# Kernel tuning notes

Measured on AMD Instinct MI355X. Metric: run time of the kernel, lower is better.

The kernel has to match this reference:

```python
import jax, jax.numpy as jnp
import numpy as np

N_SRC = 50000
N_TGT = 50000
E = 320000
D = 256          # feature dim == hidden_channels
H = 256
OUT = 16
L = 2
P_DROP = 0.1
NEG_SLOPE = 0.01  # F.leaky_relu default


def _seg_mean(x, src_idx, dst_idx, n_dst):
    # gather source features along edges, mean-aggregate per destination (PyG SAGE default aggr='mean')
    msgs = x[src_idx]                                            # [E, D]
    s = jax.ops.segment_sum(msgs, dst_idx, num_segments=n_dst)   # [n_dst, D]
    cnt = jax.ops.segment_sum(jnp.ones((dst_idx.shape[0],), x.dtype), dst_idx, num_segments=n_dst)
    return s / jnp.maximum(cnt, 1.0)[:, None]


def _dropout(x, p, key):
    keep = jax.random.bernoulli(key, 1.0 - p, x.shape)
    return jnp.where(keep, x / (1.0 - p), jnp.zeros((), x.dtype))


def setup_inputs() -> dict:
    key = jax.random.key(0)
    ks = jax.random.split(key, 16)
    sc_in = 1.0 / np.sqrt(D)
    sc_h = 1.0 / np.sqrt(H)
    inp = {
        'x_source': jax.random.normal(ks[0], (N_SRC, D), jnp.float32),
        'x_target': jax.random.normal(ks[1], (N_TGT, D), jnp.float32),
        'ei_st': jax.random.randint(ks[2], (2, E), 0, N_SRC, jnp.int32),  # row0: source idx, row1: target idx
        'ei_ts': jax.random.randint(ks[3], (2, E), 0, N_TGT, jnp.int32),  # row0: target idx, row1: source idx
        # SAGEConv params per layer per relation; lin_l has bias, lin_r does not (PyG)
        'Wl_st': jax.random.normal(ks[4], (L, D, H), jnp.float32) * sc_in,
        'Wr_st': jax.random.normal(ks[5], (L, D, H), jnp.float32) * sc_in,
        'b_st': jnp.zeros((L, H), jnp.float32),
        'Wl_ts': jax.random.normal(ks[6], (L, D, H), jnp.float32) * sc_in,
        'Wr_ts': jax.random.normal(ks[7], (L, D, H), jnp.float32) * sc_in,
        'b_ts': jnp.zeros((L, H), jnp.float32),
        'Wout': jax.random.normal(ks[8], (H, OUT), jnp.float32) * sc_h,
        'bout': jnp.zeros((OUT,), jnp.float32),
    }
    return inp


def reference(x_source, x_target, ei_st, ei_ts, Wl_st, Wr_st, b_st, Wl_ts, Wr_ts, b_ts, Wout, bout):
    drop_key = jax.random.key(42)
    x_s, x_t = x_source, x_target
    for l in range(L):
        # relation ('source','edge','target'): messages source -> target
        m_t = _seg_mean(x_s, ei_st[0], ei_st[1], N_TGT)
        new_t = m_t @ Wl_st[l] + b_st[l] + x_t @ Wr_st[l]
        # relation ('target','rev_edge','source'): messages target -> source
        m_s = _seg_mean(x_t, ei_ts[0], ei_ts[1], N_SRC)
        new_s = m_s @ Wl_ts[l] + b_ts[l] + x_s @ Wr_ts[l]
        # leaky_relu + dropout (F.dropout default training=True)
        new_s = jnp.where(new_s >= 0, new_s, NEG_SLOPE * new_s)
        new_t = jnp.where(new_t >= 0, new_t, NEG_SLOPE * new_t)
        x_s = _dropout(new_s, P_DROP, jax.random.fold_in(drop_key, 2 * l))
        x_t = _dropout(new_t, P_DROP, jax.random.fold_in(drop_key, 2 * l + 1))
    return x_s @ Wout + bout  # [N_SRC, OUT]
```

## Files before the change

### kernel.cpp

```cpp
#include <hip/hip_runtime.h>
#include <stdint.h>

#define NSRC 50000
#define NTGT 50000
#define NE   320000
#define DIN  256
#define HID  256
#define DOUT 16

#define GBM 64
#define GBLK ((NSRC + GBM - 1) / GBM)
#define MASK_DW_PER (GBLK * 512)

typedef __attribute__((ext_vector_type(8))) short bf16x8;
typedef __attribute__((ext_vector_type(4))) float f32x4;

__device__ inline ushort f2b(float f) {
  uint32_t u = __float_as_uint(f);
  return (ushort)((u + 0x7FFFu + ((u >> 16) & 1u)) >> 16);
}
__device__ inline float b2f(ushort h) { return __uint_as_float(((uint32_t)h) << 16); }

typedef __attribute__((address_space(3))) uint32_t lds_u32_t;
typedef const __attribute__((address_space(1))) uint32_t glb_u32_t;
__device__ __forceinline__ void ld_lds16(const ushort* g, ushort* lds) {
  __builtin_amdgcn_global_load_lds((glb_u32_t*)g, (lds_u32_t*)lds, 16, 0, 0);
}

__host__ __device__ constexpr uint64_t tf2x32(uint32_t k0, uint32_t k1,
                                              uint32_t x0, uint32_t x1) {
  uint32_t ks2 = k0 ^ k1 ^ 0x1BD11BDAu;
  x0 += k0; x1 += k1;
#define TF_ROT(x, r) (((x) << (r)) | ((x) >> (32 - (r))))
#define TF_RND(r) { x0 += x1; x1 = TF_ROT(x1, r) ^ x0; }
  TF_RND(13) TF_RND(15) TF_RND(26) TF_RND(6)
  x0 += k1;  x1 += ks2 + 1u;
  TF_RND(17) TF_RND(29) TF_RND(16) TF_RND(24)
  x0 += ks2; x1 += k0 + 2u;
  TF_RND(13) TF_RND(15) TF_RND(26) TF_RND(6)
  x0 += k0;  x1 += k1 + 3u;
  TF_RND(17) TF_RND(29) TF_RND(16) TF_RND(24)
  x0 += k1;  x1 += ks2 + 4u;
  TF_RND(13) TF_RND(15) TF_RND(26) TF_RND(6)
  x0 += ks2; x1 += k0 + 5u;
#undef TF_RND
#undef TF_ROT
  return (uint64_t(x0) << 32) | uint64_t(x1);
}

constexpr uint64_t FOLD[4] = {
  tf2x32(0u, 42u, 0u, 0u),
  tf2x32(0u, 42u, 0u, 1u),
  tf2x32(0u, 42u, 0u, 2u),
  tf2x32(0u, 42u, 0u, 3u),
};

__device__ __forceinline__ void mask_word(uint32_t* __restrict__ masks, int d) {
  int g = d / MASK_DW_PER;
  int w = d - g * MASK_DW_PER;
  int gt = w >> 1, half = w & 1;
  int gblk = gt >> 8, gtid = gt & 255;
  int wave = gtid >> 6, lane = gtid & 63;
  int q = lane >> 4, r = lane & 15;
  uint64_t fk = (g == 0) ? FOLD[1] : (g == 1 ? FOLD[0] : FOLD[2]);
  uint32_t kk0 = (uint32_t)(fk >> 32), kk1 = (uint32_t)fk;
  int mbase = gblk * GBM;
  uint32_t mword = 0;
#pragma unroll
  for (int bb = 0; bb < 32; ++bb) {
    int s = half * 32 + bb;
    int si = s >> 4, se = (s >> 2) & 3, sj = s & 3;
    uint32_t rowg = (uint32_t)(mbase + si * 16 + q * 4 + se);
    uint32_t colg = (uint32_t)(wave * 64 + sj * 16 + r);
    uint64_t rr = tf2x32(kk0, kk1, 0u, rowg * 256u + colg);
    uint32_t bits = (uint32_t)(rr >> 32) ^ (uint32_t)rr;
    mword |= (((bits >> 9) < 7549747u) ? 1u : 0u) << bb;
  }
  masks[d] = mword;
}

#define NB_CVT  25000
#define NB_W    96
#define NB_HIST 2500
#define PREP_T  (NB_CVT + NB_W + NB_HIST)

struct PrepArgs {
  const float *xs, *xt;
  ushort *oxs, *oxt;
  const float* wsrc[6];
  ushort* wdst[6];
  const int *ei_a, *ei_b;
  int *cur_a, *cur_b;
};

__global__ __launch_bounds__(256) void prep_kernel(PrepArgs p) {
  __shared__ ushort tile[64][65];
  int blk = (int)(((long long)blockIdx.x * 97) % PREP_T);
  int tid = threadIdx.x;
  if (blk < NB_CVT) {
    const float* in = blk < (NB_CVT / 2) ? p.xs : p.xt;
    ushort* out = blk < (NB_CVT / 2) ? p.oxs : p.oxt;
    int i = (blk % (NB_CVT / 2)) * 256 + tid;
    float4 v = ((const float4*)in)[i];
    ushort4 o;
    o.x = f2b(v.x); o.y = f2b(v.y); o.z = f2b(v.z); o.w = f2b(v.w);
    ((ushort4*)out)[i] = o;
    return;
  }
  blk -= NB_CVT;
  if (blk < NB_W) {
    const float* W = p.wsrc[blk >> 4];
    ushort* Wt = p.wdst[blk >> 4];
    int ktile = (blk >> 2) & 3, ntile = blk & 3;
#pragma unroll
    for (int rep = 0; rep < 16; ++rep) {
      int lin = rep * 256 + tid;
      int kk = lin >> 6, nn = lin & 63;
      tile[nn][kk] = f2b(W[(size_t)(ktile * 64 + kk) * 256 + ntile * 64 + nn]);
    }
    __syncthreads();
#pragma unroll
    for (int rep = 0; rep < 16; ++rep) {
      int lin = rep * 256 + tid;
      int nn = lin >> 6, kk = lin & 63;
      Wt[(size_t)(ntile * 64 + nn) * 256 + ktile * 64 + kk] = tile[nn][kk];
    }
    return;
  }
  blk -= NB_W;
  const int* ei = blk < (NB_HIST / 2) ? p.ei_a : p.ei_b;
  int* cur = blk < (NB_HIST / 2) ? p.cur_a : p.cur_b;
  int e = (blk % (NB_HIST / 2)) * 256 + tid;
  if (e < NE) atomicAdd(cur + ei[NE + e], 1);
}

#define SB 1024
__global__ __launch_bounds__(SB) void scan_partial(const int* __restrict__ cur_a,
                                                   const int* __restrict__ cur_b,
                                                   int* __restrict__ bsum,
                                                   int n, int nbPer) {
  __shared__ int red[SB];
  int b = blockIdx.x;
  const int* cnt = b < nbPer ? cur_a : cur_b;
  int i = (b % nbPer) * SB + threadIdx.x;
  red[threadIdx.x] = (i < n) ? cnt[i] : 0;
  __syncthreads();
  for (int d = SB / 2; d > 0; d >>= 1) {
    if (threadIdx.x < d) red[threadIdx.x] += red[threadIdx.x + d];
    __syncthreads();
  }
  if (threadIdx.x == 0) bsum[b] = red[0];
}

__global__ __launch_bounds__(128) void scan_base(int* __restrict__ bsum, int nbPer) {
  __shared__ int buf[2][64];
  int half = threadIdx.x >> 6;
  int t = threadIdx.x & 63;
  buf[half][t] = (t < nbPer) ? bsum[half * nbPer + t] : 0;
  __syncthreads();
  for (int d = 1; d < 64; d <<= 1) {
    int v = (t >= d) ? buf[half][t - d] : 0;
    __syncthreads();
    buf[half][t] += v;
    __syncthreads();
  }
  if (t < nbPer) bsum[half * nbPer + t] = (t == 0) ? 0 : buf[half][t - 1];
}

__global__ __launch_bounds__(SB) void scan_final(int* __restrict__ cur_a,
                                                 int* __restrict__ cur_b,
                                                 int* __restrict__ offs_a,
                                                 int* __restrict__ offs_b,
                                                 const int* __restrict__ bsum,
                                                 int n, int nbPer) {
  __shared__ int part[SB];
  int b = blockIdx.x;
  bool first = b < nbPer;
  int* cur = first ? cur_a : cur_b;
  int* offs = first ? offs_a : offs_b;
  int i = (b % nbPer) * SB + threadIdx.x;
  int v = (i < n) ? cur[i] : 0;
  part[threadIdx.x] = v;
  __syncthreads();
  for (int d = 1; d < SB; d <<= 1) {
    int tv = (threadIdx.x >= d) ? part[threadIdx.x - d] : 0;
    __syncthreads();
    part[threadIdx.x] += tv;
    __syncthreads();
  }
  int excl = part[threadIdx.x] - v + bsum[b];
  if (i < n) {
    offs[i] = excl;
    cur[i] = 0;
  }
  if (i == n - 1) offs[n] = excl + v;
}

__global__ __launch_bounds__(256) void csr_fill2(const int* __restrict__ ei_a,
                                                 const int* __restrict__ ei_b,
                                                 const int* __restrict__ offs_a,
                                                 const int* __restrict__ offs_b,
                                                 int* __restrict__ cur_a,
                                                 int* __restrict__ cur_b,
                                                 int* __restrict__ adj_a,
                                                 int* __restrict__ adj_b,
                                                 int nE, int nbPer) {
  int blk = blockIdx.x;
  bool first = blk < nbPer;
  const int* ei = first ? ei_a : ei_b;
  const int* offs = first ? offs_a : offs_b;
  int* cur = first ? cur_a : cur_b;
  int* adj = first ? adj_a : adj_b;
  int e = (blk % nbPer) * 256 + threadIdx.x;
  if (e >= nE) return;
  int dst = ei[nE + e];
  int pos = atomicAdd(cur + dst, 1);
  adj[offs[dst] + pos] = ei[e];
}

__device__ __forceinline__ void gather_row(const ushort* __restrict__ x,
                                           const int* __restrict__ offs,
                                           const int* __restrict__ adj,
                                           ushort* __restrict__ m,
                                           int row, int lane) {
  int start = offs[row], end = offs[row + 1];
  float a0 = 0.f, a1 = 0.f, a2 = 0.f, a3 = 0.f;
  int e = start;
  for (; e + 3 < end; e += 4) {
    int s0 = adj[e], s1 = adj[e + 1], s2 = adj[e + 2], s3 = adj[e + 3];
    ushort4 v0 = *(const ushort4*)(x + (size_t)s0 * DIN + lane * 4);
    ushort4 v1 = *(const ushort4*)(x + (size_t)s1 * DIN + lane * 4);
    ushort4 v2 = *(const ushort4*)(x + (size_t)s2 * DIN + lane * 4);
    ushort4 v3 = *(const ushort4*)(x + (size_t)s3 * DIN + lane * 4);
    a0 += b2f(v0.x); a1 += b2f(v0.y); a2 += b2f(v0.z); a3 += b2f(v0.w);
    a0 += b2f(v1.x); a1 += b2f(v1.y); a2 += b2f(v1.z); a3 += b2f(v1.w);
    a0 += b2f(v2.x); a1 += b2f(v2.y); a2 += b2f(v2.z); a3 += b2f(v2.w);
    a0 += b2f(v3.x); a1 += b2f(v3.y); a2 += b2f(v3.z); a3 += b2f(v3.w);
  }
  for (; e < end; ++e) {
    int s = adj[e];
    ushort4 v = *(const ushort4*)(x + (size_t)s * DIN + lane * 4);
    a0 += b2f(v.x); a1 += b2f(v.y); a2 += b2f(v.z); a3 += b2f(v.w);
  }
  float inv = 1.0f / fmaxf((float)(end - start), 1.0f);
  ushort4 o;
  o.x = f2b(a0 * inv); o.y = f2b(a1 * inv); o.z = f2b(a2 * inv); o.w = f2b(a3 * inv);
  *(ushort4*)(m + (size_t)row * DIN + lane * 4) = o;
}

#define GG_GB 12500
#define G2_MASKB (2 * MASK_DW_PER / 256)
#define G2_T (2 * GG_GB + G2_MASKB)

__global__ __launch_bounds__(256) void gather2_mean_h(
    const ushort* __restrict__ xa, const int* __restrict__ offsa,
    const int* __restrict__ adja, ushort* __restrict__ ma,
    const ushort* __restrict__ xb, const int* __restrict__ offsb,
    const int* __restrict__ adjb, ushort* __restrict__ mb,
    uint32_t* __restrict__ masks, int nRows, int nbPer) {
  int blk = (int)(((long long)blockIdx.x * 97) % G2_T);
  int tid = threadIdx.x;
  if (blk >= 2 * nbPer) {
    mask_word(masks, (blk - 2 * nbPer) * 256 + tid);
    return;
  }
  bool first = blk < nbPer;
  int row = (blk % nbPer) * 4 + (tid >> 6);
  if (row >= nRows) return;
  if (first) gather_row(xa, offsa, adja, ma, row, tid & 63);
  else       gather_row(xb, offsb, adjb, mb, row, tid & 63);
}

__device__ __forceinline__ void gemm_body(
    int bid, const ushort* __restrict__ A1, const ushort* __restrict__ A2,
    const ushort* __restrict__ W1t, const ushort* __restrict__ W2t,
    const float* __restrict__ bias, const uint2* __restrict__ mk,
    ushort* __restrict__ C, int M, ushort* sA, ushort* sB) {
  const int tid = threadIdx.x;
  const int wave = tid >> 6, lane = tid & 63;
  const int q = lane >> 4, r = lane & 15;
  const int mbase = bid * GBM;

  const uint2 km = mk[bid * 256 + tid];

  f32x4 acc[4][4] = {};

  const int arow = tid >> 2;
  const int akc = (tid & 3) * 8;
  const int agrow = min(mbase + arow, M - 1);
  const ushort* a1p = A1 + (size_t)agrow * DIN + akc;
  const ushort* a2p = A2 + (size_t)agrow * DIN + akc;
  const ushort* w1b = W1t + (size_t)arow * DIN + akc;
  const ushort* w2b = W2t + (size_t)arow * DIN + akc;
  ushort* ldsA0 = sA + wave * 512;
  ushort* ldsA1 = sA + 2048 + wave * 512;

#pragma unroll
  for (int t = 0; t < 8; ++t) {
    const int kt = t * 32;
    __syncthreads();
    ld_lds16(a1p + kt, ldsA0);
    ld_lds16(a2p + kt, ldsA1);
#pragma unroll
    for (int c = 0; c < 4; ++c) {
      ld_lds16(w1b + c * (64 * DIN) + kt, sB + c * 2048 + wave * 512);
      ld_lds16(w2b + c * (64 * DIN) + kt, sB + 8192 + c * 2048 + wave * 512);
    }
    __syncthreads();
#pragma unroll
    for (int ph = 0; ph < 2; ++ph) {
      bf16x8 af[4], bfr[4];
#pragma unroll
      for (int i = 0; i < 4; ++i)
        af[i] = *(const bf16x8*)&sA[ph * 2048 + (i * 16 + r) * 32 + q * 8];
#pragma unroll
      for (int j = 0; j < 4; ++j)
        bfr[j] = *(const bf16x8*)&sB[ph * 8192 + (wave * 64 + j * 16 + r) * 32 + q * 8];
#pragma unroll
      for (int i = 0; i < 4; ++i)
#pragma unroll
        for (int j = 0; j < 4; ++j)
          acc[i][j] = __builtin_amdgcn_mfma_f32_16x16x32_bf16(af[i], bfr[j],
                                                              acc[i][j], 0, 0, 0);
    }
  }

  float bj[4];
#pragma unroll
  for (int j = 0; j < 4; ++j) bj[j] = bias[wave * 64 + j * 16 + r];
#pragma unroll
  for (int i = 0; i < 4; ++i) {
#pragma unroll
    for (int e = 0; e < 4; ++e) {
      int rowg = mbase + i * 16 + q * 4 + e;
      if (rowg >= M) continue;
#pragma unroll
      for (int j = 0; j < 4; ++j) {
        const int s = i * 16 + e * 4 + j;
        int colg = wave * 64 + j * 16 + r;
        float v = acc[i][j][e] + bj[j];
        v = v >= 0.0f ? v : 0.01f * v;
        uint32_t keep = ((s < 32 ? km.x >> s : km.y >> (s - 32)) & 1u);
        v = keep ? v * (1.0f / 0.9f) : 0.0f;
        C[(size_t)rowg * HID + colg] = f2b(v);
      }
    }
  }
}

__global__ __launch_bounds__(256, 4) void gemm_dual_mfma(
    const ushort* __restrict__ A1, const ushort* __restrict__ A2,
    const ushort* __restrict__ W1t, const ushort* __restrict__ W2t,
    const float* __restrict__ bias, const uint2* __restrict__ mk,
    ushort* __restrict__ C, int M) {
  __shared__ ushort sA[2][GBM * 32];
  __shared__ ushort sB[2][HID * 32];
  gemm_body(blockIdx.x, A1, A2, W1t, W2t, bias, mk, C, M, &sA[0][0], &sB[0][0]);
}

#define GG_MASKB (MASK_DW_PER / 256)
#define GG_T  (GBLK + GG_GB + GG_MASKB)

__global__ __launch_bounds__(256, 4) void gemm_gather(
    const ushort* __restrict__ A1, const ushort* __restrict__ A2,
    const ushort* __restrict__ W1t, const ushort* __restrict__ W2t,
    const float* __restrict__ bias, const uint2* __restrict__ mk,
    ushort* __restrict__ C, int M,
    const ushort* __restrict__ gx, const int* __restrict__ goffs,
    const int* __restrict__ gadj, ushort* __restrict__ gm, int gRows,
    uint32_t* __restrict__ masks) {
  __shared__ ushort sA[2][GBM * 32];
  __shared__ ushort sB[2][HID * 32];
  int blk = (int)(((long long)blockIdx.x * 101) % GG_T);
  if (blk < GBLK) {
    gemm_body(blk, A1, A2, W1t, W2t, bias, mk, C, M, &sA[0][0], &sB[0][0]);
  } else if (blk < GBLK + GG_GB) {
    int row = (blk - GBLK) * 4 + (threadIdx.x >> 6);
    if (row < gRows) gather_row(gx, goffs, gadj, gm, row, threadIdx.x & 63);
  } else {
    mask_word(masks,
              2 * MASK_DW_PER + (blk - GBLK - GG_GB) * 256 + (int)threadIdx.x);
  }
}

__global__ __launch_bounds__(256) void out_gemm_h(const ushort* __restrict__ X,
                                                  const float* __restrict__ Wout,
                                                  const float* __restrict__ bout,
                                                  float* __restrict__ C, int M) {
  __shared__ float sW[DIN * DOUT];
  int tid = threadIdx.x;
#pragma unroll
  for (int i = 0; i < (DIN * DOUT) / 256; ++i) sW[i * 256 + tid] = Wout[i * 256 + tid];
  __syncthreads();
  int rr = tid >> 4, c = tid & 15;
  int row = blockIdx.x * 16 + rr;
  if (row >= M) return;
  float acc = bout[c];
  const ushort* xp = X + (size_t)row * DIN;
  for (int k = 0; k < DIN; k += 8) {
    uint4 u = *(const uint4*)(xp + k);
    const ushort* us = (const ushort*)&u;
#pragma unroll
    for (int t = 0; t < 8; ++t) acc += b2f(us[t]) * sW[(k + t) * DOUT + c];
  }
  C[(size_t)row * DOUT + c] = acc;
}

extern "C" void kernel_launch(void* const* d_in, const int* in_sizes, int n_in,
                              void* d_out, int out_size, void* d_ws, size_t ws_size,
                              hipStream_t stream) {
  const float* x_source = (const float*)d_in[0];
  const float* x_target = (const float*)d_in[1];
  const int* ei_st = (const int*)d_in[2];
  const int* ei_ts = (const int*)d_in[3];
  const float* Wl_st = (const float*)d_in[4];
  const float* Wr_st = (const float*)d_in[5];
  const float* b_st  = (const float*)d_in[6];
  const float* Wl_ts = (const float*)d_in[7];
  const float* Wr_ts = (const float*)d_in[8];
  const float* b_ts  = (const float*)d_in[9];
  const float* Wout  = (const float*)d_in[10];
  const float* bout  = (const float*)d_in[11];
  float* out = (float*)d_out;

  const size_t F = (size_t)NSRC * DIN;
  const size_t WM = (size_t)DIN * HID;
  const int nbScan = (NSRC + SB - 1) / SB;
  const size_t intCount = (NTGT + 1) + (NSRC + 1) + 2 * NE + NTGT + NSRC +
                          2 * nbScan + 3 * MASK_DW_PER;
  const size_t need = (5 * F + 6 * WM) * sizeof(ushort) + intCount * sizeof(int);
  if (ws_size < need) return;

  ushort* xs0h = (ushort*)d_ws;
  ushort* xt0h = xs0h + F;
  ushort* B0h  = xt0h + F;
  ushort* B1h  = B0h + F;
  ushort* B2h  = B1h + F;
  ushort* wt0  = B2h + F;
  ushort* wt1  = wt0 + WM;
  ushort* wt2  = wt1 + WM;
  ushort* wt3  = wt2 + WM;
  ushort* wt4  = wt3 + WM;
  ushort* wt5  = wt4 + WM;
  int* ip      = (int*)(wt5 + WM);
  int* offs_st = ip;
  int* offs_ts = offs_st + NTGT + 1;
  int* adj_st  = offs_ts + NSRC + 1;
  int* adj_ts  = adj_st + NE;
  int* cur_t   = adj_ts + NE;
  int* cur_s   = cur_t + NTGT;
  int* bsum    = cur_s + NSRC;
  uint32_t* masks = (uint32_t*)(bsum + 2 * nbScan);

  const int EB = (NE + 255) / 256;
  const int GGB = NTGT / 4;

  hipMemsetAsync(cur_t, 0, (NTGT + NSRC) * sizeof(int), stream);
  PrepArgs pa;
  pa.xs = x_source; pa.xt = x_target; pa.oxs = xs0h; pa.oxt = xt0h;
  pa.wsrc[0] = Wl_st;      pa.wdst[0] = wt0;
  pa.wsrc[1] = Wr_st;      pa.wdst[1] = wt1;
  pa.wsrc[2] = Wl_ts;      pa.wdst[2] = wt2;
  pa.wsrc[3] = Wr_ts;      pa.wdst[3] = wt3;
  pa.wsrc[4] = Wl_ts + WM; pa.wdst[4] = wt4;
  pa.wsrc[5] = Wr_ts + WM; pa.wdst[5] = wt5;
  pa.ei_a = ei_st; pa.ei_b = ei_ts;
  pa.cur_a = cur_t; pa.cur_b = cur_s;
  prep_kernel<<<PREP_T, 256, 0, stream>>>(pa);

  scan_partial<<<2 * nbScan, SB, 0, stream>>>(cur_t, cur_s, bsum, NTGT, nbScan);
  scan_base<<<1, 128, 0, stream>>>(bsum, nbScan);
  scan_final<<<2 * nbScan, SB, 0, stream>>>(cur_t, cur_s, offs_st, offs_ts,
                                            bsum, NTGT, nbScan);
  csr_fill2<<<2 * EB, 256, 0, stream>>>(ei_st, ei_ts, offs_st, offs_ts,
                                        cur_t, cur_s, adj_st, adj_ts, NE, EB);

  gather2_mean_h<<<G2_T, 256, 0, stream>>>(xs0h, offs_st, adj_st, B0h,
                                           xt0h, offs_ts, adj_ts, B1h,
                                           masks, NTGT, GGB);

  gemm_dual_mfma<<<GBLK, 256, 0, stream>>>(
      B0h, xt0h, wt0, wt1, b_st, (const uint2*)(masks), B2h, NTGT);

  gemm_gather<<<GG_T, 256, 0, stream>>>(
      B1h, xs0h, wt2, wt3, b_ts, (const uint2*)(masks + MASK_DW_PER), B0h, NSRC,
      B2h, offs_ts, adj_ts, xt0h, NSRC, masks);

  gemm_dual_mfma<<<GBLK, 256, 0, stream>>>(
      xt0h, B0h, wt4, wt5, b_ts + HID, (const uint2*)(masks + 2 * MASK_DW_PER),
      B2h, NSRC);

  out_gemm_h<<<(NSRC + 15) / 16, 256, 0, stream>>>(B2h, Wout, bout, out, NSRC);
}
```

Baseline: 446.6 us.

## Fuse output projection into final GEMM and widen gather to 16-byte loads

The final dual GEMM now applies leaky_relu and dropout, writes the activated bf16 tile to swizzled LDS, and computes the 256x16 output projection in the same kernel. This removes the separate out_gemm kernel and the global round-trip of the last hidden activations. The mean-gather now uses 32 lanes per row with 16-byte loads, so each block covers 8 rows and the grid is halved. Mask and gather outputs use nontemporal stores. The risks are higher LDS use and register pressure in the fused kernel, and fewer in-flight rows per wave in the gather.

After: 544.8 us. 22.0% more time.

```diff
diff --git a/kernel.cpp b/kernel.cpp
--- a/kernel.cpp
+++ b/kernel.cpp
@@ -14,6 +14,7 @@
 
 typedef __attribute__((ext_vector_type(8))) short bf16x8;
 typedef __attribute__((ext_vector_type(4))) float f32x4;
+typedef __attribute__((ext_vector_type(4))) uint u32x4;
 
 __device__ inline ushort f2b(float f) {
   uint32_t u = __float_as_uint(f);
@@ -76,7 +77,7 @@
     uint32_t bits = (uint32_t)(rr >> 32) ^ (uint32_t)rr;
     mword |= (((bits >> 9) < 7549747u) ? 1u : 0u) << bb;
   }
-  masks[d] = mword;
+  __builtin_nontemporal_store(mword, masks + d);
 }
 
 #define NB_CVT  25000
@@ -218,37 +219,52 @@
   adj[offs[dst] + pos] = ei[e];
 }
 
-__device__ __forceinline__ void gather_row(const ushort* __restrict__ x,
-                                           const int* __restrict__ offs,
-                                           const int* __restrict__ adj,
-                                           ushort* __restrict__ m,
-                                           int row, int lane) {
+__device__ __forceinline__ void gather_row8(const ushort* __restrict__ x,
+                                            const int* __restrict__ offs,
+                                            const int* __restrict__ adj,
+                                            ushort* __restrict__ m,
+                                            int row, int lane) {
   int start = offs[row], end = offs[row + 1];
   float a0 = 0.f, a1 = 0.f, a2 = 0.f, a3 = 0.f;
+  float a4 = 0.f, a5 = 0.f, a6 = 0.f, a7 = 0.f;
+  const ushort* xb = x + lane * 8;
   int e = start;
   for (; e + 3 < end; e += 4) {
     int s0 = adj[e], s1 = adj[e + 1], s2 = adj[e + 2], s3 = adj[e + 3];
-    ushort4 v0 = *(const ushort4*)(x + (size_t)s0 * DIN + lane * 4);
-    ushort4 v1 = *(const ushort4*)(x + (size_t)s1 * DIN + lane * 4);
-    ushort4 v2 = *(const ushort4*)(x + (size_t)s2 * DIN + lane * 4);
-    ushort4 v3 = *(const ushort4*)(x + (size_t)s3 * DIN + lane * 4);
-    a0 += b2f(v0.x); a1 += b2f(v0.y); a2 += b2f(v0.z); a3 += b2f(v0.w);
-    a0 += b2f(v1.x); a1 += b2f(v1.y); a2 += b2f(v1.z); a3 += b2f(v1.w);
-    a0 += b2f(v2.x); a1 += b2f(v2.y); a2 += b2f(v2.z); a3 += b2f(v2.w);
-    a0 += b2f(v3.x); a1 += b2f(v3.y); a2 += b2f(v3.z); a3 += b2f(v3.w);
+    u32x4 v0 = *(const u32x4*)(xb + (size_t)s0 * DIN);
+    u32x4 v1 = *(const u32x4*)(xb + (size_t)s1 * DIN);
+    u32x4 v2 = *(const u32x4*)(xb + (size_t)s2 * DIN);
+    u32x4 v3 = *(const u32x4*)(xb + (size_t)s3 * DIN);
+    const ushort* u;
+    u = (const ushort*)&v0;
+    a0 += b2f(u[0]); a1 += b2f(u[1]); a2 += b2f(u[2]); a3 += b2f(u[3]);
+    a4 += b2f(u[4]); a5 += b2f(u[5]); a6 += b2f(u[6]); a7 += b2f(u[7]);
+    u = (const ushort*)&v1;
+    a0 += b2f(u[0]); a1 += b2f(u[1]); a2 += b2f(u[2]); a3 += b2f(u[3]);
+    a4 += b2f(u[4]); a5 += b2f(u[5]); a6 += b2f(u[6]); a7 += b2f(u[7]);
+    u = (const ushort*)&v2;
+    a0 += b2f(u[0]); a1 += b2f(u[1]); a2 += b2f(u[2]); a3 += b2f(u[3]);
+    a4 += b2f(u[4]); a5 += b2f(u[5]); a6 += b2f(u[6]); a7 += b2f(u[7]);
+    u = (const ushort*)&v3;
+    a0 += b2f(u[0]); a1 += b2f(u[1]); a2 += b2f(u[2]); a3 += b2f(u[3]);
+    a4 += b2f(u[4]); a5 += b2f(u[5]); a6 += b2f(u[6]); a7 += b2f(u[7]);
   }
   for (; e < end; ++e) {
     int s = adj[e];
-    ushort4 v = *(const ushort4*)(x + (size_t)s * DIN + lane * 4);
-    a0 += b2f(v.x); a1 += b2f(v.y); a2 += b2f(v.z); a3 += b2f(v.w);
+    u32x4 v = *(const u32x4*)(xb + (size_t)s * DIN);
+    const ushort* u = (const ushort*)&v;
+    a0 += b2f(u[0]); a1 += b2f(u[1]); a2 += b2f(u[2]); a3 += b2f(u[3]);
+    a4 += b2f(u[4]); a5 += b2f(u[5]); a6 += b2f(u[6]); a7 += b2f(u[7]);
   }
   float inv = 1.0f / fmaxf((float)(end - start), 1.0f);
-  ushort4 o;
-  o.x = f2b(a0 * inv); o.y = f2b(a1 * inv); o.z = f2b(a2 * inv); o.w = f2b(a3 * inv);
-  *(ushort4*)(m + (size_t)row * DIN + lane * 4) = o;
-}
-
-#define GG_GB 12500
+  ushort o[8];
+  o[0] = f2b(a0 * inv); o[1] = f2b(a1 * inv); o[2] = f2b(a2 * inv); o[3] = f2b(a3 * inv);
+  o[4] = f2b(a4 * inv); o[5] = f2b(a5 * inv); o[6] = f2b(a6 * inv); o[7] = f2b(a7 * inv);
+  __builtin_nontemporal_store(*(const u32x4*)o,
+                              (u32x4*)(m + (size_t)row * DIN + lane * 8));
+}
+
+#define GG_GB 6250
 #define G2_MASKB (2 * MASK_DW_PER / 256)
 #define G2_T (2 * GG_GB + G2_MASKB)
 
@@ -265,10 +281,60 @@
     return;
   }
   bool first = blk < nbPer;
-  int row = (blk % nbPer) * 4 + (tid >> 6);
+  int row = (blk % nbPer) * 8 + (tid >> 5);
   if (row >= nRows) return;
-  if (first) gather_row(xa, offsa, adja, ma, row, tid & 63);
-  else       gather_row(xb, offsb, adjb, mb, row, tid & 63);
+  if (first) gather_row8(xa, offsa, adja, ma, row, tid & 31);
+  else       gather_row8(xb, offsb, adjb, mb, row, tid & 31);
+}
+
+__device__ __forceinline__ void gemm_kloop(
+    int bid, const ushort* __restrict__ A1, const ushort* __restrict__ A2,
+    const ushort* __restrict__ W1t, const ushort* __restrict__ W2t,
+    int M, ushort* sA, ushort* sB, f32x4 acc[4][4]) {
+  const int tid = threadIdx.x;
+  const int wave = tid >> 6, lane = tid & 63;
+  const int q = lane >> 4, r = lane & 15;
+  const int mbase = bid * GBM;
+
+  const int arow = tid >> 2;
+  const int akc = (tid & 3) * 8;
+  const int agrow = min(mbase + arow, M - 1);
+  const ushort* a1p = A1 + (size_t)agrow * DIN + akc;
+  const ushort* a2p = A2 + (size_t)agrow * DIN + akc;
+  const ushort* w1b = W1t + (size_t)arow * DIN + akc;
+  const ushort* w2b = W2t + (size_t)arow * DIN + akc;
+  ushort* ldsA0 = sA + wave * 512;
+  ushort* ldsA1 = sA + 2048 + wave * 512;
+
+#pragma unroll
+  for (int t = 0; t < 8; ++t) {
+    const int kt = t * 32;
+    __syncthreads();
+    ld_lds16(a1p + kt, ldsA0);
+    ld_lds16(a2p + kt, ldsA1);
+#pragma unroll
+    for (int c = 0; c < 4; ++c) {
+      ld_lds16(w1b + c * (64 * DIN) + kt, sB + c * 2048 + wave * 512);
+      ld_lds16(w2b + c * (64 * DIN) + kt, sB + 8192 + c * 2048 + wave * 512);
+    }
+    __syncthreads();
+#pragma unroll
+    for (int ph = 0; ph < 2; ++ph) {
+      bf16x8 af[4], bfr[4];
+#pragma unroll
+      for (int i = 0; i < 4; ++i)
+        af[i] = *(const bf16x8*)&sA[ph * 2048 + (i * 16 + r) * 32 + q * 8];
+#pragma unroll
+      for (int j = 0; j < 4; ++j)
+        bfr[j] = *(const bf16x8*)&sB[ph * 8192 + (wave * 64 + j * 16 + r) * 32 + q * 8];
+#pragma unroll
+      for (int i = 0; i < 4; ++i)
+#pragma unroll
+        for (int j = 0; j < 4; ++j)
+          acc[i][j] = __builtin_amdgcn_mfma_f32_16x16x32_bf16(af[i], bfr[j],
+                                                              acc[i][j], 0, 0, 0);
+    }
+  }
 }
 
 __device__ __forceinline__ void gemm_body(
@@ -280,50 +346,10 @@
   const int wave = tid >> 6, lane = tid & 63;
   const int q = lane >> 4, r = lane & 15;
   const int mbase = bid * GBM;
-
   const uint2 km = mk[bid * 256 + tid];
 
   f32x4 acc[4][4] = {};
-
-  const int arow = tid >> 2;
-  const int akc = (tid & 3) * 8;
-  const int agrow = min(mbase + arow, M - 1);
-  const ushort* a1p = A1 + (size_t)agrow * DIN + akc;
-  const ushort* a2p = A2 + (size_t)agrow * DIN + akc;
-  const ushort* w1b = W1t + (size_t)arow * DIN + akc;
-  const ushort* w2b = W2t + (size_t)arow * DIN + akc;
-  ushort* ldsA0 = sA + wave * 512;
-  ushort* ldsA1 = sA + 2048 + wave * 512;
-
-#pragma unroll
-  for (int t = 0; t < 8; ++t) {
-    const int kt = t * 32;
-    __syncthreads();
-    ld_lds16(a1p + kt, ldsA0);
-    ld_lds16(a2p + kt, ldsA1);
-#pragma unroll
-    for (int c = 0; c < 4; ++c) {
-      ld_lds16(w1b + c * (64 * DIN) + kt, sB + c * 2048 + wave * 512);
-      ld_lds16(w2b + c * (64 * DIN) + kt, sB + 8192 + c * 2048 + wave * 512);
-    }
-    __syncthreads();
-#pragma unroll
-    for (int ph = 0; ph < 2; ++ph) {
-      bf16x8 af[4], bfr[4];
-#pragma unroll
-      for (int i = 0; i < 4; ++i)
-        af[i] = *(const bf16x8*)&sA[ph * 2048 + (i * 16 + r) * 32 + q * 8];
-#pragma unroll
-      for (int j = 0; j < 4; ++j)
-        bfr[j] = *(const bf16x8*)&sB[ph * 8192 + (wave * 64 + j * 16 + r) * 32 + q * 8];
-#pragma unroll
-      for (int i = 0; i < 4; ++i)
-#pragma unroll
-        for (int j = 0; j < 4; ++j)
-          acc[i][j] = __builtin_amdgcn_mfma_f32_16x16x32_bf16(af[i], bfr[j],
-                                                              acc[i][j], 0, 0, 0);
-    }
-  }
+  gemm_kloop(bid, A1, A2, W1t, W2t, M, sA, sB, acc);
 
   float bj[4];
 #pragma unroll
@@ -375,35 +401,88 @@
   if (blk < GBLK) {
     gemm_body(blk, A1, A2, W1t, W2t, bias, mk, C, M, &sA[0][0], &sB[0][0]);
   } else if (blk < GBLK + GG_GB) {
-    int row = (blk - GBLK) * 4 + (threadIdx.x >> 6);
-    if (row < gRows) gather_row(gx, goffs, gadj, gm, row, threadIdx.x & 63);
+    int row = (blk - GBLK) * 8 + (threadIdx.x >> 5);
+    if (row < gRows) gather_row8(gx, goffs, gadj, gm, row, threadIdx.x & 31);
   } else {
     mask_word(masks,
               2 * MASK_DW_PER + (blk - GBLK - GG_GB) * 256 + (int)threadIdx.x);
   }
 }
 
-__global__ __launch_bounds__(256) void out_gemm_h(const ushort* __restrict__ X,
-                                                  const float* __restrict__ Wout,
-                                                  const float* __restrict__ bout,
-                                                  float* __restrict__ C, int M) {
-  __shared__ float sW[DIN * DOUT];
-  int tid = threadIdx.x;
-#pragma unroll
-  for (int i = 0; i < (DIN * DOUT) / 256; ++i) sW[i * 256 + tid] = Wout[i * 256 + tid];
+__global__ __launch_bounds__(256, 3) void gemm_dual_out(
+    const ushort* __restrict__ A1, const ushort* __restrict__ A2,
+    const ushort* __restrict__ W1t, const ushort* __restrict__ W2t,
+    const float* __restrict__ bias, const uint2* __restrict__ mk,
+    const float* __restrict__ Wout, const float* __restrict__ bout,
+    float* __restrict__ outp, int M) {
+  __shared__ __align__(16) ushort smem[24576];
+  ushort* sA = smem;
+  ushort* sB = smem + 4096;
+  const int tid = threadIdx.x;
+  const int wave = tid >> 6, lane = tid & 63;
+  const int q = lane >> 4, r = lane & 15;
+  const int bid = blockIdx.x;
+  const int mbase = bid * GBM;
+  const uint2 km = mk[bid * 256 + tid];
+
+  f32x4 acc[4][4] = {};
+  gemm_kloop(bid, A1, A2, W1t, W2t, M, sA, sB, acc);
+
   __syncthreads();
-  int rr = tid >> 4, c = tid & 15;
-  int row = blockIdx.x * 16 + rr;
-  if (row >= M) return;
-  float acc = bout[c];
-  const ushort* xp = X + (size_t)row * DIN;
-  for (int k = 0; k < DIN; k += 8) {
-    uint4 u = *(const uint4*)(xp + k);
+
+  float* sWt = (float*)(smem + 16384);
+#pragma unroll
+  for (int i = 0; i < 16; ++i) {
+    int idx = i * 256 + tid;
+    sWt[(idx & 15) * 256 + (idx >> 4)] = Wout[idx];
+  }
+
+  float bj[4];
+#pragma unroll
+  for (int j = 0; j < 4; ++j) bj[j] = bias[wave * 64 + j * 16 + r];
+#pragma unroll
+  for (int i = 0; i < 4; ++i) {
+#pragma unroll
+    for (int e = 0; e < 4; ++e) {
+      int rowl = i * 16 + q * 4 + e;
+#pragma unroll
+      for (int j = 0; j < 4; ++j) {
+        const int s = i * 16 + e * 4 + j;
+        int colg = wave * 64 + j * 16 + r;
+        float v = acc[i][j][e] + bj[j];
+        v = v >= 0.0f ? v : 0.01f * v;
+        uint32_t keep = ((s < 32 ? km.x >> s : km.y >> (s - 32)) & 1u);
+        v = keep ? v * (1.0f / 0.9f) : 0.0f;
+        int byte = (rowl * 512 + colg * 2) ^ ((rowl & 7) << 4);
+        *(ushort*)((char*)smem + byte) = f2b(v);
+      }
+    }
+  }
+  __syncthreads();
+
+  int rowl = tid & 63, c0 = (tid >> 6) * 4;
+  int rowg = mbase + rowl;
+  float o0 = bout[c0], o1 = bout[c0 + 1], o2 = bout[c0 + 2], o3 = bout[c0 + 3];
+  const int sw = (rowl & 7) << 4;
+#pragma unroll
+  for (int k8 = 0; k8 < 32; ++k8) {
+    u32x4 u = *(const u32x4*)((char*)smem + ((rowl * 512 + k8 * 16) ^ sw));
     const ushort* us = (const ushort*)&u;
 #pragma unroll
-    for (int t = 0; t < 8; ++t) acc += b2f(us[t]) * sW[(k + t) * DOUT + c];
-  }
-  C[(size_t)row * DOUT + c] = acc;
+    for (int t = 0; t < 8; ++t) {
+      float f = b2f(us[t]);
+      int k = k8 * 8 + t;
+      o0 += f * sWt[(c0 + 0) * 256 + k];
+      o1 += f * sWt[(c0 + 1) * 256 + k];
+      o2 += f * sWt[(c0 + 2) * 256 + k];
+      o3 += f * sWt[(c0 + 3) * 256 + k];
+    }
+  }
+  if (rowg < M) {
+    o0 += 0.0f; o1 += 0.0f; o2 += 0.0f; o3 += 0.0f;
+    float* op = outp + (size_t)rowg * DOUT + c0;
+    op[0] = o0; op[1] = o1; op[2] = o2; op[3] = o3;
+  }
 }
 
 extern "C" void kernel_launch(void* const* d_in, const int* in_sizes, int n_in,
@@ -453,7 +532,7 @@
   uint32_t* masks = (uint32_t*)(bsum + 2 * nbScan);
 
   const int EB = (NE + 255) / 256;
-  const int GGB = NTGT / 4;
+  const int GGB = NTGT / 8;
 
   hipMemsetAsync(cur_t, 0, (NTGT + NSRC) * sizeof(int), stream);
   PrepArgs pa;
@@ -486,9 +565,7 @@
       B1h, xs0h, wt2, wt3, b_ts, (const uint2*)(masks + MASK_DW_PER), B0h, NSRC,
       B2h, offs_ts, adj_ts, xt0h, NSRC, masks);
 
-  gemm_dual_mfma<<<GBLK, 256, 0, stream>>>(
+  gemm_dual_out<<<GBLK, 256, 0, stream>>>(
       xt0h, B0h, wt4, wt5, b_ts + HID, (const uint2*)(masks + 2 * MASK_DW_PER),
-      B2h, NSRC);
-
-  out_gemm_h<<<(NSRC + 15) / 16, 256, 0, stream>>>(B2h, Wout, bout, out, NSRC);
-}
+      Wout, bout, out, NSRC);
+}
```

## Widen gather to 16-byte loads and overlap second gather with first GEMM

Applied to the files above, without the earlier changes.

The mean-gather now uses 32 lanes per row, with each lane loading 8 bf16 values (16 bytes) per neighbor, so one block covers 8 rows instead of 4. The second layer-0 gather, which has no dependence on the first GEMM, moves out of the combined gather kernel and is co-scheduled inside a new fused GEMM+gather launch. The intent is wider memory transactions and better overlap of memory-bound gather with compute-bound GEMM. The trade-off is fewer active lanes per row and more register pressure from eight accumulators.

New measurement: 442.2 us. About the same (-1.0%).

```diff
diff --git a/kernel.cpp b/kernel.cpp
--- a/kernel.cpp
+++ b/kernel.cpp
@@ -14,6 +14,7 @@
 
 typedef __attribute__((ext_vector_type(8))) short bf16x8;
 typedef __attribute__((ext_vector_type(4))) float f32x4;
+typedef __attribute__((ext_vector_type(4))) uint u32x4;
 
 __device__ inline ushort f2b(float f) {
   uint32_t u = __float_as_uint(f);
@@ -218,57 +219,116 @@
   adj[offs[dst] + pos] = ei[e];
 }
 
-__device__ __forceinline__ void gather_row(const ushort* __restrict__ x,
-                                           const int* __restrict__ offs,
-                                           const int* __restrict__ adj,
-                                           ushort* __restrict__ m,
-                                           int row, int lane) {
+__device__ __forceinline__ void gather_row8(const ushort* __restrict__ x,
+                                            const int* __restrict__ offs,
+                                            const int* __restrict__ adj,
+                                            ushort* __restrict__ m,
+                                            int row, int lane) {
   int start = offs[row], end = offs[row + 1];
   float a0 = 0.f, a1 = 0.f, a2 = 0.f, a3 = 0.f;
+  float a4 = 0.f, a5 = 0.f, a6 = 0.f, a7 = 0.f;
+  const ushort* xb = x + lane * 8;
   int e = start;
   for (; e + 3 < end; e += 4) {
     int s0 = adj[e], s1 = adj[e + 1], s2 = adj[e + 2], s3 = adj[e + 3];
-    ushort4 v0 = *(const ushort4*)(x + (size_t)s0 * DIN + lane * 4);
-    ushort4 v1 = *(const ushort4*)(x + (size_t)s1 * DIN + lane * 4);
-    ushort4 v2 = *(const ushort4*)(x + (size_t)s2 * DIN + lane * 4);
-    ushort4 v3 = *(const ushort4*)(x + (size_t)s3 * DIN + lane * 4);
-    a0 += b2f(v0.x); a1 += b2f(v0.y); a2 += b2f(v0.z); a3 += b2f(v0.w);
-    a0 += b2f(v1.x); a1 += b2f(v1.y); a2 += b2f(v1.z); a3 += b2f(v1.w);
-    a0 += b2f(v2.x); a1 += b2f(v2.y); a2 += b2f(v2.z); a3 += b2f(v2.w);
-    a0 += b2f(v3.x); a1 += b2f(v3.y); a2 += b2f(v3.z); a3 += b2f(v3.w);
+    u32x4 v0 = *(const u32x4*)(xb + (size_t)s0 * DIN);
+    u32x4 v1 = *(const u32x4*)(xb + (size_t)s1 * DIN);
+    u32x4 v2 = *(const u32x4*)(xb + (size_t)s2 * DIN);
+    u32x4 v3 = *(const u32x4*)(xb + (size_t)s3 * DIN);
+    const ushort* u;
+    u = (const ushort*)&v0;
+    a0 += b2f(u[0]); a1 += b2f(u[1]); a2 += b2f(u[2]); a3 += b2f(u[3]);
+    a4 += b2f(u[4]); a5 += b2f(u[5]); a6 += b2f(u[6]); a7 += b2f(u[7]);
+    u = (const ushort*)&v1;
+    a0 += b2f(u[0]); a1 += b2f(u[1]); a2 += b2f(u[2]); a3 += b2f(u[3]);
+    a4 += b2f(u[4]); a5 += b2f(u[5]); a6 += b2f(u[6]); a7 += b2f(u[7]);
+    u = (const ushort*)&v2;
+    a0 += b2f(u[0]); a1 += b2f(u[1]); a2 += b2f(u[2]); a3 += b2f(u[3]);
+    a4 += b2f(u[4]); a5 += b2f(u[5]); a6 += b2f(u[6]); a7 += b2f(u[7]);
+    u = (const ushort*)&v3;
+    a0 += b2f(u[0]); a1 += b2f(u[1]); a2 += b2f(u[2]); a3 += b2f(u[3]);
+    a4 += b2f(u[4]); a5 += b2f(u[5]); a6 += b2f(u[6]); a7 += b2f(u[7]);
   }
   for (; e < end; ++e) {
     int s = adj[e];
-    ushort4 v = *(const ushort4*)(x + (size_t)s * DIN + lane * 4);
-    a0 += b2f(v.x); a1 += b2f(v.y); a2 += b2f(v.z); a3 += b2f(v.w);
+    u32x4 v = *(const u32x4*)(xb + (size_t)s * DIN);
+    const ushort* u = (const ushort*)&v;
+    a0 += b2f(u[0]); a1 += b2f(u[1]); a2 += b2f(u[2]); a3 += b2f(u[3]);
+    a4 += b2f(u[4]); a5 += b2f(u[5]); a6 += b2f(u[6]); a7 += b2f(u[7]);
   }
   float inv = 1.0f / fmaxf((float)(end - start), 1.0f);
-  ushort4 o;
-  o.x = f2b(a0 * inv); o.y = f2b(a1 * inv); o.z = f2b(a2 * inv); o.w = f2b(a3 * inv);
-  *(ushort4*)(m + (size_t)row * DIN + lane * 4) = o;
-}
-
-#define GG_GB 12500
+  ushort o[8];
+  o[0] = f2b(a0 * inv); o[1] = f2b(a1 * inv); o[2] = f2b(a2 * inv); o[3] = f2b(a3 * inv);
+  o[4] = f2b(a4 * inv); o[5] = f2b(a5 * inv); o[6] = f2b(a6 * inv); o[7] = f2b(a7 * inv);
+  *(u32x4*)(m + (size_t)row * DIN + lane * 8) = *(const u32x4*)o;
+}
+
+#define GG_GB 6250
 #define G2_MASKB (2 * MASK_DW_PER / 256)
-#define G2_T (2 * GG_GB + G2_MASKB)
-
-__global__ __launch_bounds__(256) void gather2_mean_h(
-    const ushort* __restrict__ xa, const int* __restrict__ offsa,
-    const int* __restrict__ adja, ushort* __restrict__ ma,
-    const ushort* __restrict__ xb, const int* __restrict__ offsb,
-    const int* __restrict__ adjb, ushort* __restrict__ mb,
-    uint32_t* __restrict__ masks, int nRows, int nbPer) {
-  int blk = (int)(((long long)blockIdx.x * 97) % G2_T);
+#define GM_T (GG_GB + G2_MASKB)
+
+__global__ __launch_bounds__(256) void gather_mask_h(
+    const ushort* __restrict__ x, const int* __restrict__ offs,
+    const int* __restrict__ adj, ushort* __restrict__ m,
+    uint32_t* __restrict__ masks, int nRows) {
+  int blk = (int)(((long long)blockIdx.x * 97) % GM_T);
   int tid = threadIdx.x;
-  if (blk >= 2 * nbPer) {
-    mask_word(masks, (blk - 2 * nbPer) * 256 + tid);
+  if (blk >= GG_GB) {
+    mask_word(masks, (blk - GG_GB) * 256 + tid);
     return;
   }
-  bool first = blk < nbPer;
-  int row = (blk % nbPer) * 4 + (tid >> 6);
-  if (row >= nRows) return;
-  if (first) gather_row(xa, offsa, adja, ma, row, tid & 63);
-  else       gather_row(xb, offsb, adjb, mb, row, tid & 63);
+  int row = blk * 8 + (tid >> 5);
+  if (row < nRows) gather_row8(x, offs, adj, m, row, tid & 31);
+}
+
+__device__ __forceinline__ void gemm_kloop(
+    int bid, const ushort* __restrict__ A1, const ushort* __restrict__ A2,
+    const ushort* __restrict__ W1t, const ushort* __restrict__ W2t,
+    int M, ushort* sA, ushort* sB, f32x4 acc[4][4]) {
+  const int tid = threadIdx.x;
+  const int wave = tid >> 6, lane = tid & 63;
+  const int q = lane >> 4, r = lane & 15;
+  const int mbase = bid * GBM;
+
+  const int arow = tid >> 2;
+  const int akc = (tid & 3) * 8;
+  const int agrow = min(mbase + arow, M - 1);
+  const ushort* a1p = A1 + (size_t)agrow * DIN + akc;
+  const ushort* a2p = A2 + (size_t)agrow * DIN + akc;
+  const ushort* w1b = W1t + (size_t)arow * DIN + akc;
+  const ushort* w2b = W2t + (size_t)arow * DIN + akc;
+  ushort* ldsA0 = sA + wave * 512;
+  ushort* ldsA1 = sA + 2048 + wave * 512;
+
+#pragma unroll
+  for (int t = 0; t < 8; ++t) {
+    const int kt = t * 32;
+    __syncthreads();
+    ld_lds16(a1p + kt, ldsA0);
+    ld_lds16(a2p + kt, ldsA1);
+#pragma unroll
+    for (int c = 0; c < 4; ++c) {
+      ld_lds16(w1b + c * (64 * DIN) + kt, sB + c * 2048 + wave * 512);
+      ld_lds16(w2b + c * (64 * DIN) + kt, sB + 8192 + c * 2048 + wave * 512);
+    }
+    __syncthreads();
+#pragma unroll
+    for (int ph = 0; ph < 2; ++ph) {
+      bf16x8 af[4], bfr[4];
+#pragma unroll
+      for (int i = 0; i < 4; ++i)
+        af[i] = *(const bf16x8*)&sA[ph * 2048 + (i * 16 + r) * 32 + q * 8];
+#pragma unroll
+      for (int j = 0; j < 4; ++j)
+        bfr[j] = *(const bf16x8*)&sB[ph * 8192 + (wave * 64 + j * 16 + r) * 32 + q * 8];
+#pragma unroll
+      for (int i = 0; i < 4; ++i)
+#pragma unroll
+        for (int j = 0; j < 4; ++j)
+          acc[i][j] = __builtin_amdgcn_mfma_f32_16x16x32_bf16(af[i], bfr[j],
+                                                              acc[i][j], 0, 0, 0);
+    }
+  }
 }
 
 __device__ __forceinline__ void gemm_body(
@@ -280,50 +340,10 @@
   const int wave = tid >> 6, lane = tid & 63;
   const int q = lane >> 4, r = lane & 15;
   const int mbase = bid * GBM;
-
   const uint2 km = mk[bid * 256 + tid];
 
   f32x4 acc[4][4] = {};
-
-  const int arow = tid >> 2;
-  const int akc = (tid & 3) * 8;
-  const int agrow = min(mbase + arow, M - 1);
-  const ushort* a1p = A1 + (size_t)agrow * DIN + akc;
-  const ushort* a2p = A2 + (size_t)agrow * DIN + akc;
-  const ushort* w1b = W1t + (size_t)arow * DIN + akc;
-  const ushort* w2b = W2t + (size_t)arow * DIN + akc;
-  ushort* ldsA0 = sA + wave * 512;
-  ushort* ldsA1 = sA + 2048 + wave * 512;
-
-#pragma unroll
-  for (int t = 0; t < 8; ++t) {
-    const int kt = t * 32;
-    __syncthreads();
-    ld_lds16(a1p + kt, ldsA0);
-    ld_lds16(a2p + kt, ldsA1);
-#pragma unroll
-    for (int c = 0; c < 4; ++c) {
-      ld_lds16(w1b + c * (64 * DIN) + kt, sB + c * 2048 + wave * 512);
-      ld_lds16(w2b + c * (64 * DIN) + kt, sB + 8192 + c * 2048 + wave * 512);
-    }
-    __syncthreads();
-#pragma unroll
-    for (int ph = 0; ph < 2; ++ph) {
-      bf16x8 af[4], bfr[4];
-#pragma unroll
-      for (int i = 0; i < 4; ++i)
-        af[i] = *(const bf16x8*)&sA[ph * 2048 + (i * 16 + r) * 32 + q * 8];
-#pragma unroll
-      for (int j = 0; j < 4; ++j)
-        bfr[j] = *(const bf16x8*)&sB[ph * 8192 + (wave * 64 + j * 16 + r) * 32 + q * 8];
-#pragma unroll
-      for (int i = 0; i < 4; ++i)
-#pragma unroll
-        for (int j = 0; j < 4; ++j)
-          acc[i][j] = __builtin_amdgcn_mfma_f32_16x16x32_bf16(af[i], bfr[j],
-                                                              acc[i][j], 0, 0, 0);
-    }
-  }
+  gemm_kloop(bid, A1, A2, W1t, W2t, M, sA, sB, acc);
 
   float bj[4];
 #pragma unroll
@@ -356,6 +376,26 @@
   __shared__ ushort sA[2][GBM * 32];
   __shared__ ushort sB[2][HID * 32];
   gemm_body(blockIdx.x, A1, A2, W1t, W2t, bias, mk, C, M, &sA[0][0], &sB[0][0]);
+}
+
+#define G1_T (GBLK + GG_GB)
+
+__global__ __launch_bounds__(256, 4) void gemm1_gather(
+    const ushort* __restrict__ A1, const ushort* __restrict__ A2,
+    const ushort* __restrict__ W1t, const ushort* __restrict__ W2t,
+    const float* __restrict__ bias, const uint2* __restrict__ mk,
+    ushort* __restrict__ C, int M,
+    const ushort* __restrict__ gx, const int* __restrict__ goffs,
+    const int* __restrict__ gadj, ushort* __restrict__ gm, int gRows) {
+  __shared__ ushort sA[2][GBM * 32];
+  __shared__ ushort sB[2][HID * 32];
+  int blk = (int)(((long long)blockIdx.x * 101) % G1_T);
+  if (blk < GBLK) {
+    gemm_body(blk, A1, A2, W1t, W2t, bias, mk, C, M, &sA[0][0], &sB[0][0]);
+  } else {
+    int row = (blk - GBLK) * 8 + (threadIdx.x >> 5);
+    if (row < gRows) gather_row8(gx, goffs, gadj, gm, row, threadIdx.x & 31);
+  }
 }
 
 #define GG_MASKB (MASK_DW_PER / 256)
@@ -375,8 +415,8 @@
   if (blk < GBLK) {
     gemm_body(blk, A1, A2, W1t, W2t, bias, mk, C, M, &sA[0][0], &sB[0][0]);
   } else if (blk < GBLK + GG_GB) {
-    int row = (blk - GBLK) * 4 + (threadIdx.x >> 6);
-    if (row < gRows) gather_row(gx, goffs, gadj, gm, row, threadIdx.x & 63);
+    int row = (blk - GBLK) * 8 + (threadIdx.x >> 5);
+    if (row < gRows) gather_row8(gx, goffs, gadj, gm, row, threadIdx.x & 31);
   } else {
     mask_word(masks,
               2 * MASK_DW_PER + (blk - GBLK - GG_GB) * 256 + (int)threadIdx.x);
@@ -453,9 +493,8 @@
   uint32_t* masks = (uint32_t*)(bsum + 2 * nbScan);
 
   const int EB = (NE + 255) / 256;
-  const int GGB = NTGT / 4;
-
-  hipMemsetAsync(cur_t, 0, (NTGT + NSRC) * sizeof(int), stream);
+
+  (void)hipMemsetAsync(cur_t, 0, (NTGT + NSRC) * sizeof(int), stream);
   PrepArgs pa;
   pa.xs = x_source; pa.xt = x_target; pa.oxs = xs0h; pa.oxt = xt0h;
   pa.wsrc[0] = Wl_st;      pa.wdst[0] = wt0;
@@ -475,12 +514,12 @@
   csr_fill2<<<2 * EB, 256, 0, stream>>>(ei_st, ei_ts, offs_st, offs_ts,
                                         cur_t, cur_s, adj_st, adj_ts, NE, EB);
 
-  gather2_mean_h<<<G2_T, 256, 0, stream>>>(xs0h, offs_st, adj_st, B0h,
-                                           xt0h, offs_ts, adj_ts, B1h,
-                                           masks, NTGT, GGB);
-
-  gemm_dual_mfma<<<GBLK, 256, 0, stream>>>(
-      B0h, xt0h, wt0, wt1, b_st, (const uint2*)(masks), B2h, NTGT);
+  gather_mask_h<<<GM_T, 256, 0, stream>>>(xs0h, offs_st, adj_st, B0h,
+                                          masks, NTGT);
+
+  gemm1_gather<<<G1_T, 256, 0, stream>>>(
+      B0h, xt0h, wt0, wt1, b_st, (const uint2*)(masks), B2h, NTGT,
+      xt0h, offs_ts, adj_ts, B1h, NSRC);
 
   gemm_gather<<<GG_T, 256, 0, stream>>>(
       B1h, xs0h, wt2, wt3, b_ts, (const uint2*)(masks + MASK_DW_PER), B0h, NSRC,
```
